# Performance work log

Hardware: AMD Instinct MI355X
Metric: run time of the kernel (lower is better)

Reference implementation:

```python
import jax, jax.numpy as jnp
import numpy as np

N, M, F, W = 600000, 300000, 128, 256  # points, masked points, grid feat_dim, net width


def _lin_init(k, fi, fo):
    k1, k2 = jax.random.split(k)
    s = 1.0 / np.sqrt(fi)
    return (jax.random.uniform(k1, (fi, fo), jnp.float32, -s, s),
            jax.random.uniform(k2, (fo,), jnp.float32, -s, s))


def setup_inputs() -> dict:
    key = jax.random.key(0)
    ks = jax.random.split(key, 24)
    # unique sorted indices emulate the boolean target_mask (static count M)
    idx = jnp.asarray(np.sort(np.random.RandomState(0).permutation(N)[:M]).astype(np.int32))
    inp = {
        "rays_pts_emb": jax.random.normal(ks[0], (N, 3), jnp.float32),
        "rotations_emb": jax.random.normal(ks[1], (N, 4), jnp.float32),
        "shs_emb": jax.random.normal(ks[2], (N, 16, 3), jnp.float32),
        "time_emb": jax.random.uniform(ks[3], (N, 1), jnp.float32),
        "h_emb": jax.random.uniform(ks[4], (N, 1), jnp.float32),
        "grid_sp": jax.random.normal(ks[5], (M, F), jnp.float32),
        "grid_st": jax.random.normal(ks[6], (M, F), jnp.float32),
        "idx": idx,
    }
    layers = [("sp", F, W), ("st", F, W), ("p1", W, W), ("p2", W, 9),
              ("r1", W, W), ("r2", W, 4), ("s1", W, W), ("s2", W, 48),
              ("w1", W, W), ("w2", W, 1), ("m1", W, W), ("m2", W, 1)]
    for i, (nm, fi, fo) in enumerate(layers):
        Wt, b = _lin_init(ks[7 + i], fi, fo)
        inp["W_" + nm] = Wt
        inp["b_" + nm] = b
    return inp


def _head(x, W1, b1, W2, b2):
    # nn.Sequential(ReLU, Linear, ReLU, Linear)
    h = jax.nn.relu(x)
    h = jax.nn.relu(h @ W1 + b1)
    return h @ W2 + b2


def reference(rays_pts_emb, rotations_emb, shs_emb, time_emb, h_emb, grid_sp, grid_st, idx,
              W_sp, b_sp, W_st, b_st, W_p1, b_p1, W_p2, b_p2, W_r1, b_r1, W_r2, b_r2,
              W_s1, b_s1, W_s2, b_s2, W_w1, b_w1, W_w2, b_w2, W_m1, b_m1, W_m2, b_m2):
    # encoders (Linear only, no activation)
    sp = grid_sp @ W_sp + b_sp            # [M, W]
    st = grid_st @ W_st + b_st            # [M, W]
    t = time_emb[0:1]                     # [1, 1]
    mint = 1.0 - t
    # position deformation: Bezier combination of 3 control offsets
    dx = _head(sp, W_p1, b_p1, W_p2, b_p2).reshape(-1, 3, 3)  # [M, 3, 3]
    delta = (3.0 * mint ** 2 * t * dx[:, 0]
             + 3.0 * mint * t ** 2 * dx[:, 1]
             + t ** 3 * dx[:, 2])                              # [M, 3]
    pts = rays_pts_emb.at[idx].add(delta)
    rotations = rotations_emb.at[idx].add(_head(st, W_r1, b_r1, W_r2, b_r2))
    shs = shs_emb.at[idx].add(_head(st, W_s1, b_s1, W_s2, b_s2).reshape(-1, 16, 3))
    # opacity gating
    w = _head(sp, W_w1, b_w1, W_w2, b_w2) ** 2                 # [M, 1]
    mu = jax.nn.sigmoid(_head(sp, W_m1, b_m1, W_m2, b_m2))     # [M, 1]
    opacity = h_emb.at[idx].set(h_emb[idx] * jnp.exp(-w * (t - mu) ** 2))
    return (pts, rotations, opacity, shs)
```

## Files before the change

### kernel.cpp

```cpp
#include <hip/hip_runtime.h>
#include <hip/hip_bf16.h>
#include <stdint.h>

#define M_ROWS 300000

typedef __attribute__((ext_vector_type(8)))  short bf16x8;
typedef __attribute__((ext_vector_type(16))) float f32x16;

union U4 { uint4 u; bf16x8 h; unsigned short us[8]; };

__device__ __forceinline__ unsigned short f2bf(float f) {
  union { float f; uint32_t u; } v; v.f = f;
  uint32_t r = v.u + 0x7fffu + ((v.u >> 16) & 1u);
  return (unsigned short)(r >> 16);
}

#define T_SP 0
#define T_ST 64
#define T_P1 128
#define T_P2 256
#define T_R1 272
#define T_R2 400
#define T_S1 416
#define T_S2 544
#define T_W1 576
#define T_W2 704
#define T_M1 720
#define T_M2 848
#define T_TOT 864

__global__ void prep_w(const float* Wsp, const float* Wst, const float* Wp1, const float* Wp2,
                       const float* Wr1, const float* Wr2, const float* Ws1, const float* Ws2,
                       const float* Ww1, const float* Ww2, const float* Wm1, const float* Wm2,
                       uint4* ws) {
  int b = blockIdx.x, l = threadIdx.x;
  const int starts[12] = {T_SP,T_ST,T_P1,T_P2,T_R1,T_R2,T_S1,T_S2,T_W1,T_W2,T_M1,T_M2};
  const int Ks[12]     = {128,128,256,256,256,256,256,256,256,256,256,256};
  const int Cos[12]    = {256,256,256,9,256,4,256,48,256,1,256,1};
  const float* Wp[12]  = {Wsp,Wst,Wp1,Wp2,Wr1,Wr2,Ws1,Ws2,Ww1,Ww2,Wm1,Wm2};
  int m = 0;
  #pragma unroll
  for (int i = 1; i < 12; ++i) if (b >= starts[i]) m = i;
  int local = b - starts[m];
  int KT = Ks[m] >> 4;
  int n0 = local / KT, k0 = local - n0 * KT;
  int col = n0 * 32 + (l & 31);
  int kbase = k0 * 16 + (l >> 5) * 8;
  const float* W = Wp[m];
  int Co = Cos[m];
  U4 pk;
  #pragma unroll
  for (int j = 0; j < 8; ++j) {
    float v = (col < Co) ? W[(size_t)(kbase + j) * Co + col] : 0.0f;
    pk.us[j] = f2bf(v);
  }
  ws[(size_t)b * 64 + l] = pk.u;
}

__global__ void copy_emb(const float4* pts, const float4* rot, const float4* h,
                         const float4* shs, float4* out) {
  long long stride = (long long)gridDim.x * blockDim.x;
  for (long long i = (long long)blockIdx.x * blockDim.x + threadIdx.x; i < 8400000LL; i += stride) {
    float4 v;
    if (i < 450000)        v = pts[i];
    else if (i < 1050000)  v = rot[i - 450000];
    else if (i < 1200000)  v = h[i - 1050000];
    else                   v = shs[i - 1200000];
    out[i] = v;
  }
}

#define LSTR 512
__device__ __forceinline__ int lds_addr(int row, int cb) {
  return row * LSTR + (cb ^ ((row & 15) << 4));
}

__device__ __forceinline__ void loadX(const float* grid, int row0, int t, char* buf) {
  #pragma unroll
  for (int i = 0; i < 4; ++i) {
    int fi = i * 512 + t;
    int row = fi >> 5;
    int c4 = fi & 31;
    int gr = row0 + row; gr = gr < M_ROWS ? gr : (M_ROWS - 1);
    float4 v = ((const float4*)grid)[(size_t)gr * 32 + c4];
    ushort4 p;
    p.x = f2bf(v.x); p.y = f2bf(v.y); p.z = f2bf(v.z); p.w = f2bf(v.w);
    *(ushort4*)(buf + lds_addr(row, c4 * 8)) = p;
  }
}

__device__ __forceinline__ void pre8(U4 (&d)[8], const uint4* base, int lane) {
  #pragma unroll
  for (int i = 0; i < 8; ++i) d[i].u = base[(size_t)i * 64 + lane];
}
__device__ __forceinline__ void pre4(U4 (&d)[8], const uint4* base, int lane) {
  #pragma unroll
  for (int i = 0; i < 4; ++i) d[i].u = base[(size_t)i * 64 + lane];
}
__device__ __forceinline__ void pre_s2(U4 (&d)[8], const uint4* wt, int kq, int lane) {
  #pragma unroll
  for (int kk = 0; kk < 4; ++kk)
    #pragma unroll
    for (int n = 0; n < 2; ++n)
      d[kk * 2 + n].u = wt[(size_t)((n * 16 + kq * 4 + kk) * 64) + lane];
}

__device__ __forceinline__ void mm_big8(U4 (&b)[8], const char* inb, int k0, int arow, int khalf,
                                        f32x16& acc0, f32x16& acc1) {
  #pragma unroll
  for (int k = 0; k < 8; ++k) {
    bf16x8 a0 = *(const bf16x8*)(inb + lds_addr(arow, (k0 + k) * 32 + khalf));
    bf16x8 a1 = *(const bf16x8*)(inb + lds_addr(32 + arow, (k0 + k) * 32 + khalf));
    acc0 = __builtin_amdgcn_mfma_f32_32x32x16_bf16(a0, b[k].h, acc0, 0, 0, 0);
    acc1 = __builtin_amdgcn_mfma_f32_32x32x16_bf16(a1, b[k].h, acc1, 0, 0, 0);
  }
}

__device__ __forceinline__ void store_act(char* outb, const float* bias, int wave, int lane,
                                          const f32x16& acc0, const f32x16& acc1) {
  const int col = wave * 32 + (lane & 31);
  const float bv = bias[col];
  #pragma unroll
  for (int q = 0; q < 16; ++q) {
    int row = (q & 3) + 8 * (q >> 2) + 4 * (lane >> 5);
    float v0 = acc0[q] + bv; v0 = fmaxf(v0, 0.0f);
    float v1 = acc1[q] + bv; v1 = fmaxf(v1, 0.0f);
    *(unsigned short*)(outb + lds_addr(row, col * 2)) = f2bf(v0);
    *(unsigned short*)(outb + lds_addr(32 + row, col * 2)) = f2bf(v1);
  }
}

__device__ __forceinline__ void mm_head1(U4 (&b)[8], const char* inb, int rg, int kq, int khalf,
                                         int lane, f32x16& acc) {
  const int arow = rg * 32 + (lane & 31);
  #pragma unroll
  for (int kk = 0; kk < 4; ++kk) {
    bf16x8 a = *(const bf16x8*)(inb + lds_addr(arow, (kq * 4 + kk) * 32 + khalf));
    acc = __builtin_amdgcn_mfma_f32_32x32x16_bf16(a, b[kk].h, acc, 0, 0, 0);
  }
}
__device__ __forceinline__ void mm_head2(U4 (&b)[8], const char* inb, int rg, int kq, int khalf,
                                         int lane, f32x16& acc0, f32x16& acc1) {
  const int arow = rg * 32 + (lane & 31);
  #pragma unroll
  for (int kk = 0; kk < 4; ++kk) {
    bf16x8 a = *(const bf16x8*)(inb + lds_addr(arow, (kq * 4 + kk) * 32 + khalf));
    acc0 = __builtin_amdgcn_mfma_f32_32x32x16_bf16(a, b[kk * 2 + 0].h, acc0, 0, 0, 0);
    acc1 = __builtin_amdgcn_mfma_f32_32x32x16_bf16(a, b[kk * 2 + 1].h, acc1, 0, 0, 0);
  }
}

template<int COLS>
__device__ __forceinline__ void head_atomic(float* outsm, int rg, int lane, const f32x16& acc) {
  int col = lane & 31;
  if (col < COLS) {
    #pragma unroll
    for (int q = 0; q < 16; ++q) {
      int row = rg * 32 + (q & 3) + 8 * (q >> 2) + 4 * (lane >> 5);
      atomicAdd(&outsm[row * COLS + col], acc[q]);
    }
  }
}
__device__ __forceinline__ void head_atomic48(float* outsm, int rg, int lane,
                                              const f32x16& a0, const f32x16& a1) {
  int c = lane & 31;
  #pragma unroll
  for (int q = 0; q < 16; ++q) {
    int row = rg * 32 + (q & 3) + 8 * (q >> 2) + 4 * (lane >> 5);
    atomicAdd(&outsm[row * 48 + c], a0[q]);
    if (c < 16) atomicAdd(&outsm[row * 48 + 32 + c], a1[q]);
  }
}

__global__ void __launch_bounds__(512, 4) deform_main(
    const float* grid_sp, const float* grid_st, const int* idx,
    const float* rays, const float* rotq, const float* shs_in,
    const float* time_emb, const float* h_emb,
    const uint4* ws,
    const float* b_sp, const float* b_st, const float* b_p1, const float* b_p2,
    const float* b_r1, const float* b_r2, const float* b_s1, const float* b_s2,
    const float* b_w1, const float* b_w2, const float* b_m1, const float* b_m2,
    float* out) {
  __shared__ char bufA[32768];
  __shared__ char bufB[32768];
  __shared__ float sm[3456];
  float* dxb  = sm;
  float* shsb = sm;
  float* wb   = sm + 3072;
  float* mub  = sm + 3136;
  float* rotb = sm + 3200;

  const int t = threadIdx.x;
  const int lane = t & 63;
  const int wave = t >> 6;
  const int rg = wave & 1;
  const int kq = wave >> 1;
  const int arow = lane & 31;
  const int khalf = (lane >> 5) * 16;
  const int row0 = blockIdx.x * 64;
  const float tt = time_emb[0];

  U4 b0[8], b1[8];
  pre8(b0, ws + (size_t)(T_SP + wave * 8) * 64, lane);

  for (int i = t; i < 576; i += 512) dxb[i] = 0.0f;
  for (int i = 3072 + t; i < 3456; i += 512) sm[i] = 0.0f;
  loadX(grid_sp, row0, t, bufA);
  __syncthreads();

  {
    f32x16 a0 = (f32x16)0.0f, a1 = (f32x16)0.0f;
    pre8(b1, ws + (size_t)(T_P1 + wave * 16) * 64, lane);
    mm_big8(b0, bufA, 0, arow, khalf, a0, a1);
    store_act(bufB, b_sp, wave, lane, a0, a1);
  }
  __syncthreads();

  {
    f32x16 a0 = (f32x16)0.0f, a1 = (f32x16)0.0f;
    pre8(b0, ws + (size_t)(T_P1 + wave * 16 + 8) * 64, lane);
    mm_big8(b1, bufB, 0, arow, khalf, a0, a1);
    pre4(b1, ws + (size_t)(T_P2 + kq * 4) * 64, lane);
    mm_big8(b0, bufB, 8, arow, khalf, a0, a1);
    store_act(bufA, b_p1, wave, lane, a0, a1);
  }
  __syncthreads();

  {
    f32x16 hacc = (f32x16)0.0f;
    pre8(b0, ws + (size_t)(T_W1 + wave * 16) * 64, lane);
    mm_head1(b1, bufA, rg, kq, khalf, lane, hacc);
    head_atomic<9>(dxb, rg, lane, hacc);
  }
  __syncthreads();

  {
    f32x16 a0 = (f32x16)0.0f, a1 = (f32x16)0.0f;
    pre8(b1, ws + (size_t)(T_W1 + wave * 16 + 8) * 64, lane);
    mm_big8(b0, bufB, 0, arow, khalf, a0, a1);
    pre4(b0, ws + (size_t)(T_W2 + kq * 4) * 64, lane);
    mm_big8(b1, bufB, 8, arow, khalf, a0, a1);
    store_act(bufA, b_w1, wave, lane, a0, a1);
  }
  __syncthreads();

  {
    f32x16 hacc = (f32x16)0.0f;
    pre8(b1, ws + (size_t)(T_M1 + wave * 16) * 64, lane);
    mm_head1(b0, bufA, rg, kq, khalf, lane, hacc);
    head_atomic<1>(wb, rg, lane, hacc);
  }
  __syncthreads();

  {
    f32x16 a0 = (f32x16)0.0f, a1 = (f32x16)0.0f;
    pre8(b0, ws + (size_t)(T_M1 + wave * 16 + 8) * 64, lane);
    mm_big8(b1, bufB, 0, arow, khalf, a0, a1);
    pre4(b1, ws + (size_t)(T_M2 + kq * 4) * 64, lane);
    mm_big8(b0, bufB, 8, arow, khalf, a0, a1);
    store_act(bufA, b_m1, wave, lane, a0, a1);
  }
  __syncthreads();

  {
    f32x16 hacc = (f32x16)0.0f;
    pre8(b0, ws + (size_t)(T_ST + wave * 8) * 64, lane);
    mm_head1(b1, bufA, rg, kq, khalf, lane, hacc);
    head_atomic<1>(mub, rg, lane, hacc);
  }
  __syncthreads();

  loadX(grid_st, row0, t, bufA);
  if (t < 256) {
    int row = t >> 2, sub = t & 3;
    int gr = row0 + row;
    if (gr < M_ROWS) {
      int g = idx[gr];
      if (sub < 3) {
        float mt = 1.0f - tt;
        float c0 = 3.0f * mt * mt * tt, c1 = 3.0f * mt * tt * tt, c2 = tt * tt * tt;
        float d0 = dxb[row * 9 + sub]     + b_p2[sub];
        float d1 = dxb[row * 9 + 3 + sub] + b_p2[3 + sub];
        float d2 = dxb[row * 9 + 6 + sub] + b_p2[6 + sub];
        out[(size_t)g * 3 + sub] = rays[(size_t)g * 3 + sub] + (c0 * d0 + c1 * d1 + c2 * d2);
      } else {
        float wr = wb[row] + b_w2[0];
        float mr = mub[row] + b_m2[0];
        float mu = 1.0f / (1.0f + expf(-mr));
        float dtm = tt - mu;
        out[4200000 + (size_t)g] = h_emb[g] * expf(-(wr * wr) * dtm * dtm);
      }
    }
  }
  __syncthreads();

  {
    f32x16 a0 = (f32x16)0.0f, a1 = (f32x16)0.0f;
    pre8(b1, ws + (size_t)(T_R1 + wave * 16) * 64, lane);
    mm_big8(b0, bufA, 0, arow, khalf, a0, a1);
    store_act(bufB, b_st, wave, lane, a0, a1);
  }
  __syncthreads();

  {
    f32x16 a0 = (f32x16)0.0f, a1 = (f32x16)0.0f;
    pre8(b0, ws + (size_t)(T_R1 + wave * 16 + 8) * 64, lane);
    mm_big8(b1, bufB, 0, arow, khalf, a0, a1);
    pre4(b1, ws + (size_t)(T_R2 + kq * 4) * 64, lane);
    mm_big8(b0, bufB, 8, arow, khalf, a0, a1);
    store_act(bufA, b_r1, wave, lane, a0, a1);
  }
  __syncthreads();

  {
    f32x16 hacc = (f32x16)0.0f;
    pre8(b0, ws + (size_t)(T_S1 + wave * 16) * 64, lane);
    mm_head1(b1, bufA, rg, kq, khalf, lane, hacc);
    for (int i = t; i < 3072; i += 512) shsb[i] = 0.0f;
    head_atomic<4>(rotb, rg, lane, hacc);
  }
  __syncthreads();

  {
    f32x16 a0 = (f32x16)0.0f, a1 = (f32x16)0.0f;
    pre8(b1, ws + (size_t)(T_S1 + wave * 16 + 8) * 64, lane);
    mm_big8(b0, bufB, 0, arow, khalf, a0, a1);
    pre_s2(b0, ws + (size_t)T_S2 * 64, kq, lane);
    mm_big8(b1, bufB, 8, arow, khalf, a0, a1);
    store_act(bufA, b_s1, wave, lane, a0, a1);
    if (t < 256) {
      int row = t >> 2, c = t & 3;
      int gr = row0 + row;
      if (gr < M_ROWS) {
        int g = idx[gr];
        out[1800000 + (size_t)g * 4 + c] = rotq[(size_t)g * 4 + c] + rotb[row * 4 + c] + b_r2[c];
      }
    }
  }
  __syncthreads();

  {
    f32x16 h0 = (f32x16)0.0f, h1 = (f32x16)0.0f;
    mm_head2(b0, bufA, rg, kq, khalf, lane, h0, h1);
    head_atomic48(shsb, rg, lane, h0, h1);
  }
  __syncthreads();

  #pragma unroll
  for (int i = 0; i < 6; ++i) {
    int e = i * 512 + t;
    int row = e / 48;
    int c = e - row * 48;
    int gr = row0 + row;
    if (gr < M_ROWS) {
      int g = idx[gr];
      out[4800000 + (size_t)g * 48 + c] = shs_in[(size_t)g * 48 + c] + shsb[e] + b_s2[c];
    }
  }
}

extern "C" void kernel_launch(void* const* d_in, const int* in_sizes, int n_in,
                              void* d_out, int out_size, void* d_ws, size_t ws_size,
                              hipStream_t stream) {
  const float* rays     = (const float*)d_in[0];
  const float* rotq     = (const float*)d_in[1];
  const float* shs      = (const float*)d_in[2];
  const float* time_emb = (const float*)d_in[3];
  const float* h_emb    = (const float*)d_in[4];
  const float* grid_sp  = (const float*)d_in[5];
  const float* grid_st  = (const float*)d_in[6];
  const int*   idx      = (const int*)d_in[7];
  uint4* ws = (uint4*)d_ws;

  prep_w<<<T_TOT, 64, 0, stream>>>(
      (const float*)d_in[8],  (const float*)d_in[10], (const float*)d_in[12], (const float*)d_in[14],
      (const float*)d_in[16], (const float*)d_in[18], (const float*)d_in[20], (const float*)d_in[22],
      (const float*)d_in[24], (const float*)d_in[26], (const float*)d_in[28], (const float*)d_in[30],
      ws);

  copy_emb<<<2048, 256, 0, stream>>>((const float4*)rays, (const float4*)rotq,
                                     (const float4*)h_emb, (const float4*)shs, (float4*)d_out);

  deform_main<<<(M_ROWS + 63) / 64, 512, 0, stream>>>(
      grid_sp, grid_st, idx, rays, rotq, shs, time_emb, h_emb, ws,
      (const float*)d_in[9],  (const float*)d_in[11], (const float*)d_in[13], (const float*)d_in[15],
      (const float*)d_in[17], (const float*)d_in[19], (const float*)d_in[21], (const float*)d_in[23],
      (const float*)d_in[25], (const float*)d_in[27], (const float*)d_in[29], (const float*)d_in[31],
      (float*)d_out);
}
```

Measured before the change: 802.1 us.

## Fuse width-1 opacity heads into hidden-layer epilogue and vectorize scatter writes

```diff
diff --git a/kernel.cpp b/kernel.cpp
--- a/kernel.cpp
+++ b/kernel.cpp
@@ -130,65 +130,45 @@
   }
 }
 
-__device__ __forceinline__ void mm_head1(U4 (&b)[8], const char* inb, int rg, int kq, int khalf,
-                                         int lane, f32x16& acc) {
+__device__ __forceinline__ f32x16 mm_head1(U4 (&b)[8], const char* inb, int rg, int kq, int khalf,
+                                           int lane) {
   const int arow = rg * 32 + (lane & 31);
-  #pragma unroll
-  for (int kk = 0; kk < 4; ++kk) {
-    bf16x8 a = *(const bf16x8*)(inb + lds_addr(arow, (kq * 4 + kk) * 32 + khalf));
-    acc = __builtin_amdgcn_mfma_f32_32x32x16_bf16(a, b[kk].h, acc, 0, 0, 0);
-  }
-}
-__device__ __forceinline__ void mm_head2(U4 (&b)[8], const char* inb, int rg, int kq, int khalf,
-                                         int lane, f32x16& acc0, f32x16& acc1) {
-  const int arow = rg * 32 + (lane & 31);
-  #pragma unroll
-  for (int kk = 0; kk < 4; ++kk) {
-    bf16x8 a = *(const bf16x8*)(inb + lds_addr(arow, (kq * 4 + kk) * 32 + khalf));
-    acc0 = __builtin_amdgcn_mfma_f32_32x32x16_bf16(a, b[kk * 2 + 0].h, acc0, 0, 0, 0);
-    acc1 = __builtin_amdgcn_mfma_f32_32x32x16_bf16(a, b[kk * 2 + 1].h, acc1, 0, 0, 0);
-  }
-}
-
-template<int COLS>
-__device__ __forceinline__ void head_atomic(float* outsm, int rg, int lane, const f32x16& acc) {
-  int col = lane & 31;
-  if (col < COLS) {
-    #pragma unroll
-    for (int q = 0; q < 16; ++q) {
-      int row = rg * 32 + (q & 3) + 8 * (q >> 2) + 4 * (lane >> 5);
-      atomicAdd(&outsm[row * COLS + col], acc[q]);
-    }
-  }
-}
-__device__ __forceinline__ void head_atomic48(float* outsm, int rg, int lane,
-                                              const f32x16& a0, const f32x16& a1) {
-  int c = lane & 31;
-  #pragma unroll
-  for (int q = 0; q < 16; ++q) {
-    int row = rg * 32 + (q & 3) + 8 * (q >> 2) + 4 * (lane >> 5);
-    atomicAdd(&outsm[row * 48 + c], a0[q]);
-    if (c < 16) atomicAdd(&outsm[row * 48 + 32 + c], a1[q]);
-  }
+  f32x16 hA = (f32x16)0.0f, hB = (f32x16)0.0f;
+  bf16x8 a0 = *(const bf16x8*)(inb + lds_addr(arow, (kq * 4 + 0) * 32 + khalf));
+  bf16x8 a1 = *(const bf16x8*)(inb + lds_addr(arow, (kq * 4 + 1) * 32 + khalf));
+  bf16x8 a2 = *(const bf16x8*)(inb + lds_addr(arow, (kq * 4 + 2) * 32 + khalf));
+  bf16x8 a3 = *(const bf16x8*)(inb + lds_addr(arow, (kq * 4 + 3) * 32 + khalf));
+  hA = __builtin_amdgcn_mfma_f32_32x32x16_bf16(a0, b[0].h, hA, 0, 0, 0);
+  hB = __builtin_amdgcn_mfma_f32_32x32x16_bf16(a1, b[1].h, hB, 0, 0, 0);
+  hA = __builtin_amdgcn_mfma_f32_32x32x16_bf16(a2, b[2].h, hA, 0, 0, 0);
+  hB = __builtin_amdgcn_mfma_f32_32x32x16_bf16(a3, b[3].h, hB, 0, 0, 0);
+  return hA + hB;
+}
+
+__device__ __forceinline__ float red32(float v) {
+  v += __shfl_xor(v, 1);  v += __shfl_xor(v, 2);  v += __shfl_xor(v, 4);
+  v += __shfl_xor(v, 8);  v += __shfl_xor(v, 16);
+  return v;
 }
 
 __global__ void __launch_bounds__(512, 4) deform_main(
     const float* grid_sp, const float* grid_st, const int* idx,
     const float* rays, const float* rotq, const float* shs_in,
     const float* time_emb, const float* h_emb,
-    const uint4* ws,
+    const uint4* ws, const float* Ww2f, const float* Wm2f,
     const float* b_sp, const float* b_st, const float* b_p1, const float* b_p2,
     const float* b_r1, const float* b_r2, const float* b_s1, const float* b_s2,
     const float* b_w1, const float* b_w2, const float* b_m1, const float* b_m2,
     float* out) {
   __shared__ char bufA[32768];
   __shared__ char bufB[32768];
-  __shared__ float sm[3456];
-  float* dxb  = sm;
+  __shared__ float sm[3584];
+  __shared__ int sidx[64];
   float* shsb = sm;
-  float* wb   = sm + 3072;
-  float* mub  = sm + 3136;
-  float* rotb = sm + 3200;
+  float* dxp  = sm;
+  float* wp   = sm + 2304;
+  float* mup  = sm + 2816;
+  float* rotb = sm + 3328;
 
   const int t = threadIdx.x;
   const int lane = t & 63;
@@ -203,15 +183,17 @@
   U4 b0[8], b1[8];
   pre8(b0, ws + (size_t)(T_SP + wave * 8) * 64, lane);
 
-  for (int i = t; i < 576; i += 512) dxb[i] = 0.0f;
-  for (int i = 3072 + t; i < 3456; i += 512) sm[i] = 0.0f;
+  if (t < 64) { int gr = row0 + t; sidx[t] = idx[gr < M_ROWS ? gr : (M_ROWS - 1)]; }
+  if (t < 256) rotb[t] = 0.0f;
   loadX(grid_sp, row0, t, bufA);
   __syncthreads();
 
   {
     f32x16 a0 = (f32x16)0.0f, a1 = (f32x16)0.0f;
     pre8(b1, ws + (size_t)(T_P1 + wave * 16) * 64, lane);
+    __builtin_amdgcn_s_setprio(1);
     mm_big8(b0, bufA, 0, arow, khalf, a0, a1);
+    __builtin_amdgcn_s_setprio(0);
     store_act(bufB, b_sp, wave, lane, a0, a1);
   }
   __syncthreads();
@@ -219,54 +201,78 @@
   {
     f32x16 a0 = (f32x16)0.0f, a1 = (f32x16)0.0f;
     pre8(b0, ws + (size_t)(T_P1 + wave * 16 + 8) * 64, lane);
+    __builtin_amdgcn_s_setprio(1);
     mm_big8(b1, bufB, 0, arow, khalf, a0, a1);
+    __builtin_amdgcn_s_setprio(0);
     pre4(b1, ws + (size_t)(T_P2 + kq * 4) * 64, lane);
+    __builtin_amdgcn_s_setprio(1);
     mm_big8(b0, bufB, 8, arow, khalf, a0, a1);
+    __builtin_amdgcn_s_setprio(0);
     store_act(bufA, b_p1, wave, lane, a0, a1);
   }
   __syncthreads();
 
   {
-    f32x16 hacc = (f32x16)0.0f;
     pre8(b0, ws + (size_t)(T_W1 + wave * 16) * 64, lane);
-    mm_head1(b1, bufA, rg, kq, khalf, lane, hacc);
-    head_atomic<9>(dxb, rg, lane, hacc);
+    f32x16 h = mm_head1(b1, bufA, rg, kq, khalf, lane);
+    int col = lane & 31;
+    if (col < 9) {
+      #pragma unroll
+      for (int q = 0; q < 16; ++q) {
+        int row = rg * 32 + (q & 3) + 8 * (q >> 2) + 4 * (lane >> 5);
+        dxp[(kq * 64 + row) * 9 + col] = h[q];
+      }
+    }
   }
   __syncthreads();
 
   {
     f32x16 a0 = (f32x16)0.0f, a1 = (f32x16)0.0f;
     pre8(b1, ws + (size_t)(T_W1 + wave * 16 + 8) * 64, lane);
+    __builtin_amdgcn_s_setprio(1);
     mm_big8(b0, bufB, 0, arow, khalf, a0, a1);
-    pre4(b0, ws + (size_t)(T_W2 + kq * 4) * 64, lane);
+    __builtin_amdgcn_s_setprio(0);
+    pre8(b0, ws + (size_t)(T_M1 + wave * 16) * 64, lane);
+    __builtin_amdgcn_s_setprio(1);
     mm_big8(b1, bufB, 8, arow, khalf, a0, a1);
-    store_act(bufA, b_w1, wave, lane, a0, a1);
-  }
-  __syncthreads();
-
-  {
-    f32x16 hacc = (f32x16)0.0f;
-    pre8(b1, ws + (size_t)(T_M1 + wave * 16) * 64, lane);
-    mm_head1(b0, bufA, rg, kq, khalf, lane, hacc);
-    head_atomic<1>(wb, rg, lane, hacc);
-  }
-  __syncthreads();
-
-  {
-    f32x16 a0 = (f32x16)0.0f, a1 = (f32x16)0.0f;
-    pre8(b0, ws + (size_t)(T_M1 + wave * 16 + 8) * 64, lane);
-    mm_big8(b1, bufB, 0, arow, khalf, a0, a1);
-    pre4(b1, ws + (size_t)(T_M2 + kq * 4) * 64, lane);
-    mm_big8(b0, bufB, 8, arow, khalf, a0, a1);
-    store_act(bufA, b_m1, wave, lane, a0, a1);
-  }
-  __syncthreads();
-
-  {
-    f32x16 hacc = (f32x16)0.0f;
+    __builtin_amdgcn_s_setprio(0);
+    const int hcol = wave * 32 + (lane & 31);
+    const float bv = b_w1[hcol], wv = Ww2f[hcol];
+    #pragma unroll
+    for (int q = 0; q < 16; ++q) {
+      int row = (q & 3) + 8 * (q >> 2) + 4 * (lane >> 5);
+      float s0 = red32(fmaxf(a0[q] + bv, 0.0f) * wv);
+      float s1 = red32(fmaxf(a1[q] + bv, 0.0f) * wv);
+      if ((lane & 31) == 0) { wp[wave * 64 + row] = s0; wp[wave * 64 + 32 + row] = s1; }
+    }
+  }
+  __syncthreads();
+
+  float pr = 0.0f, hv = 0.0f;
+  {
+    if (t < 256) {
+      int row = t >> 2, sub = t & 3;
+      int g = sidx[row];
+      if (sub < 3) pr = rays[(size_t)g * 3 + sub]; else hv = h_emb[g];
+    }
+    f32x16 a0 = (f32x16)0.0f, a1 = (f32x16)0.0f;
+    pre8(b1, ws + (size_t)(T_M1 + wave * 16 + 8) * 64, lane);
+    __builtin_amdgcn_s_setprio(1);
+    mm_big8(b0, bufB, 0, arow, khalf, a0, a1);
+    __builtin_amdgcn_s_setprio(0);
     pre8(b0, ws + (size_t)(T_ST + wave * 8) * 64, lane);
-    mm_head1(b1, bufA, rg, kq, khalf, lane, hacc);
-    head_atomic<1>(mub, rg, lane, hacc);
+    __builtin_amdgcn_s_setprio(1);
+    mm_big8(b1, bufB, 8, arow, khalf, a0, a1);
+    __builtin_amdgcn_s_setprio(0);
+    const int hcol = wave * 32 + (lane & 31);
+    const float bv = b_m1[hcol], wv = Wm2f[hcol];
+    #pragma unroll
+    for (int q = 0; q < 16; ++q) {
+      int row = (q & 3) + 8 * (q >> 2) + 4 * (lane >> 5);
+      float s0 = red32(fmaxf(a0[q] + bv, 0.0f) * wv);
+      float s1 = red32(fmaxf(a1[q] + bv, 0.0f) * wv);
+      if ((lane & 31) == 0) { mup[wave * 64 + row] = s0; mup[wave * 64 + 32 + row] = s1; }
+    }
   }
   __syncthreads();
 
@@ -275,20 +281,24 @@
     int row = t >> 2, sub = t & 3;
     int gr = row0 + row;
     if (gr < M_ROWS) {
-      int g = idx[gr];
+      int g = sidx[row];
       if (sub < 3) {
         float mt = 1.0f - tt;
         float c0 = 3.0f * mt * mt * tt, c1 = 3.0f * mt * tt * tt, c2 = tt * tt * tt;
-        float d0 = dxb[row * 9 + sub]     + b_p2[sub];
-        float d1 = dxb[row * 9 + 3 + sub] + b_p2[3 + sub];
-        float d2 = dxb[row * 9 + 6 + sub] + b_p2[6 + sub];
-        out[(size_t)g * 3 + sub] = rays[(size_t)g * 3 + sub] + (c0 * d0 + c1 * d1 + c2 * d2);
+        float d0 = b_p2[sub],     d1 = b_p2[3 + sub], d2 = b_p2[6 + sub];
+        #pragma unroll
+        for (int k = 0; k < 4; ++k) {
+          const float* dp = &dxp[(k * 64 + row) * 9];
+          d0 += dp[sub]; d1 += dp[3 + sub]; d2 += dp[6 + sub];
+        }
+        out[(size_t)g * 3 + sub] = pr + (c0 * d0 + c1 * d1 + c2 * d2);
       } else {
-        float wr = wb[row] + b_w2[0];
-        float mr = mub[row] + b_m2[0];
+        float wr = b_w2[0], mr = b_m2[0];
+        #pragma unroll
+        for (int w8 = 0; w8 < 8; ++w8) { wr += wp[w8 * 64 + row]; mr += mup[w8 * 64 + row]; }
         float mu = 1.0f / (1.0f + expf(-mr));
         float dtm = tt - mu;
-        out[4200000 + (size_t)g] = h_emb[g] * expf(-(wr * wr) * dtm * dtm);
+        out[4200000 + (size_t)g] = hv * expf(-(wr * wr) * dtm * dtm);
       }
     }
   }
@@ -297,7 +307,9 @@
   {
     f32x16 a0 = (f32x16)0.0f, a1 = (f32x16)0.0f;
     pre8(b1, ws + (size_t)(T_R1 + wave * 16) * 64, lane);
+    __builtin_amdgcn_s_setprio(1);
     mm_big8(b0, bufA, 0, arow, khalf, a0, a1);
+    __builtin_amdgcn_s_setprio(0);
     store_act(bufB, b_st, wave, lane, a0, a1);
   }
   __syncthreads();
@@ -305,56 +317,100 @@
   {
     f32x16 a0 = (f32x16)0.0f, a1 = (f32x16)0.0f;
     pre8(b0, ws + (size_t)(T_R1 + wave * 16 + 8) * 64, lane);
+    __builtin_amdgcn_s_setprio(1);
     mm_big8(b1, bufB, 0, arow, khalf, a0, a1);
+    __builtin_amdgcn_s_setprio(0);
     pre4(b1, ws + (size_t)(T_R2 + kq * 4) * 64, lane);
+    __builtin_amdgcn_s_setprio(1);
     mm_big8(b0, bufB, 8, arow, khalf, a0, a1);
+    __builtin_amdgcn_s_setprio(0);
     store_act(bufA, b_r1, wave, lane, a0, a1);
   }
   __syncthreads();
 
-  {
-    f32x16 hacc = (f32x16)0.0f;
+  float4 rq;
+  {
+    if (t < 64) rq = ((const float4*)rotq)[sidx[t]];
     pre8(b0, ws + (size_t)(T_S1 + wave * 16) * 64, lane);
-    mm_head1(b1, bufA, rg, kq, khalf, lane, hacc);
-    for (int i = t; i < 3072; i += 512) shsb[i] = 0.0f;
-    head_atomic<4>(rotb, rg, lane, hacc);
+    f32x16 h = mm_head1(b1, bufA, rg, kq, khalf, lane);
+    int col = lane & 31;
+    if (col < 4) {
+      #pragma unroll
+      for (int q = 0; q < 16; ++q) {
+        int row = rg * 32 + (q & 3) + 8 * (q >> 2) + 4 * (lane >> 5);
+        atomicAdd(&rotb[row * 4 + col], h[q]);
+      }
+    }
   }
   __syncthreads();
 
   {
     f32x16 a0 = (f32x16)0.0f, a1 = (f32x16)0.0f;
     pre8(b1, ws + (size_t)(T_S1 + wave * 16 + 8) * 64, lane);
+    __builtin_amdgcn_s_setprio(1);
     mm_big8(b0, bufB, 0, arow, khalf, a0, a1);
+    __builtin_amdgcn_s_setprio(0);
     pre_s2(b0, ws + (size_t)T_S2 * 64, kq, lane);
+    __builtin_amdgcn_s_setprio(1);
     mm_big8(b1, bufB, 8, arow, khalf, a0, a1);
+    __builtin_amdgcn_s_setprio(0);
     store_act(bufA, b_s1, wave, lane, a0, a1);
+    #pragma unroll
+    for (int i = 0; i < 6; ++i) shsb[i * 512 + t] = 0.0f;
+    if (t < 64 && row0 + t < M_ROWS) {
+      int g = sidx[t];
+      float4 o;
+      o.x = rq.x + rotb[t * 4 + 0] + b_r2[0];
+      o.y = rq.y + rotb[t * 4 + 1] + b_r2[1];
+      o.z = rq.z + rotb[t * 4 + 2] + b_r2[2];
+      o.w = rq.w + rotb[t * 4 + 3] + b_r2[3];
+      ((float4*)out)[450000 + (size_t)g] = o;
+    }
+  }
+  __syncthreads();
+
+  float4 sv0, sv1;
+  int r0v = t / 12, c40 = t - r0v * 12;
+  int e1 = 512 + t, r1v = e1 / 12, c41 = e1 - r1v * 12;
+  {
+    sv0 = ((const float4*)shs_in)[(size_t)sidx[r0v] * 12 + c40];
+    if (t < 256) sv1 = ((const float4*)shs_in)[(size_t)sidx[r1v] * 12 + c41];
+    f32x16 h0 = (f32x16)0.0f, h1 = (f32x16)0.0f;
+    const int ar = rg * 32 + (lane & 31);
+    #pragma unroll
+    for (int kk = 0; kk < 4; ++kk) {
+      bf16x8 a = *(const bf16x8*)(bufA + lds_addr(ar, (kq * 4 + kk) * 32 + khalf));
+      h0 = __builtin_amdgcn_mfma_f32_32x32x16_bf16(a, b0[kk * 2 + 0].h, h0, 0, 0, 0);
+      h1 = __builtin_amdgcn_mfma_f32_32x32x16_bf16(a, b0[kk * 2 + 1].h, h1, 0, 0, 0);
+    }
+    int c = lane & 31;
+    #pragma unroll
+    for (int q = 0; q < 16; ++q) {
+      int row = rg * 32 + (q & 3) + 8 * (q >> 2) + 4 * (lane >> 5);
+      atomicAdd(&shsb[row * 48 + c], h0[q]);
+      if (c < 16) atomicAdd(&shsb[row * 48 + 32 + c], h1[q]);
+    }
+  }
+  __syncthreads();
+
+  {
+    float4 bias0 = ((const float4*)b_s2)[c40];
+    float4 acc0 = ((const float4*)shsb)[r0v * 12 + c40];
+    if (row0 + r0v < M_ROWS) {
+      float4 o;
+      o.x = sv0.x + acc0.x + bias0.x; o.y = sv0.y + acc0.y + bias0.y;
+      o.z = sv0.z + acc0.z + bias0.z; o.w = sv0.w + acc0.w + bias0.w;
+      ((float4*)out)[1200000 + (size_t)sidx[r0v] * 12 + c40] = o;
+    }
     if (t < 256) {
-      int row = t >> 2, c = t & 3;
-      int gr = row0 + row;
-      if (gr < M_ROWS) {
-        int g = idx[gr];
-        out[1800000 + (size_t)g * 4 + c] = rotq[(size_t)g * 4 + c] + rotb[row * 4 + c] + b_r2[c];
+      float4 bias1 = ((const float4*)b_s2)[c41];
+      float4 acc1 = ((const float4*)shsb)[r1v * 12 + c41];
+      if (row0 + r1v < M_ROWS) {
+        float4 o;
+        o.x = sv1.x + acc1.x + bias1.x; o.y = sv1.y + acc1.y + bias1.y;
+        o.z = sv1.z + acc1.z + bias1.z; o.w = sv1.w + acc1.w + bias1.w;
+        ((float4*)out)[1200000 + (size_t)sidx[r1v] * 12 + c41] = o;
       }
-    }
-  }
-  __syncthreads();
-
-  {
-    f32x16 h0 = (f32x16)0.0f, h1 = (f32x16)0.0f;
-    mm_head2(b0, bufA, rg, kq, khalf, lane, h0, h1);
-    head_atomic48(shsb, rg, lane, h0, h1);
-  }
-  __syncthreads();
-
-  #pragma unroll
-  for (int i = 0; i < 6; ++i) {
-    int e = i * 512 + t;
-    int row = e / 48;
-    int c = e - row * 48;
-    int gr = row0 + row;
-    if (gr < M_ROWS) {
-      int g = idx[gr];
-      out[4800000 + (size_t)g * 48 + c] = shs_in[(size_t)g * 48 + c] + shsb[e] + b_s2[c];
     }
   }
 }
@@ -383,6 +439,7 @@
 
   deform_main<<<(M_ROWS + 63) / 64, 512, 0, stream>>>(
       grid_sp, grid_st, idx, rays, rotq, shs, time_emb, h_emb, ws,
+      (const float*)d_in[26], (const float*)d_in[30],
       (const float*)d_in[9],  (const float*)d_in[11], (const float*)d_in[13], (const float*)d_in[15],
       (const float*)d_in[17], (const float*)d_in[19], (const float*)d_in[21], (const float*)d_in[23],
       (const float*)d_in[25], (const float*)d_in[27], (const float*)d_in[29], (const float*)d_in[31],
```

Result: slower. 1.094 ms (+36.4%).

## Split sp and st branches into separate blocks with prefetched gathers

Applied to the files above, without the earlier changes.

```diff
diff --git a/kernel.cpp b/kernel.cpp
--- a/kernel.cpp
+++ b/kernel.cpp
@@ -139,16 +139,6 @@
     acc = __builtin_amdgcn_mfma_f32_32x32x16_bf16(a, b[kk].h, acc, 0, 0, 0);
   }
 }
-__device__ __forceinline__ void mm_head2(U4 (&b)[8], const char* inb, int rg, int kq, int khalf,
-                                         int lane, f32x16& acc0, f32x16& acc1) {
-  const int arow = rg * 32 + (lane & 31);
-  #pragma unroll
-  for (int kk = 0; kk < 4; ++kk) {
-    bf16x8 a = *(const bf16x8*)(inb + lds_addr(arow, (kq * 4 + kk) * 32 + khalf));
-    acc0 = __builtin_amdgcn_mfma_f32_32x32x16_bf16(a, b[kk * 2 + 0].h, acc0, 0, 0, 0);
-    acc1 = __builtin_amdgcn_mfma_f32_32x32x16_bf16(a, b[kk * 2 + 1].h, acc1, 0, 0, 0);
-  }
-}
 
 template<int COLS>
 __device__ __forceinline__ void head_atomic(float* outsm, int rg, int lane, const f32x16& acc) {
@@ -183,12 +173,13 @@
     float* out) {
   __shared__ char bufA[32768];
   __shared__ char bufB[32768];
-  __shared__ float sm[3456];
-  float* dxb  = sm;
-  float* shsb = sm;
-  float* wb   = sm + 3072;
-  float* mub  = sm + 3136;
-  float* rotb = sm + 3200;
+  __shared__ float smf[3456];
+  __shared__ int sidx[64];
+  float* dxb  = smf;
+  float* shsb = smf;
+  float* wb   = smf + 3072;
+  float* mub  = smf + 3136;
+  float* rotb = smf + 3200;
 
   const int t = threadIdx.x;
   const int lane = t & 63;
@@ -197,164 +188,200 @@
   const int kq = wave >> 1;
   const int arow = lane & 31;
   const int khalf = (lane >> 5) * 16;
-  const int row0 = blockIdx.x * 64;
+  const int path = blockIdx.x & 1;
+  const int row0 = (blockIdx.x >> 1) * 64;
   const float tt = time_emb[0];
 
   U4 b0[8], b1[8];
-  pre8(b0, ws + (size_t)(T_SP + wave * 8) * 64, lane);
-
-  for (int i = t; i < 576; i += 512) dxb[i] = 0.0f;
-  for (int i = 3072 + t; i < 3456; i += 512) sm[i] = 0.0f;
-  loadX(grid_sp, row0, t, bufA);
-  __syncthreads();
-
-  {
-    f32x16 a0 = (f32x16)0.0f, a1 = (f32x16)0.0f;
-    pre8(b1, ws + (size_t)(T_P1 + wave * 16) * 64, lane);
-    mm_big8(b0, bufA, 0, arow, khalf, a0, a1);
-    store_act(bufB, b_sp, wave, lane, a0, a1);
-  }
-  __syncthreads();
-
-  {
-    f32x16 a0 = (f32x16)0.0f, a1 = (f32x16)0.0f;
-    pre8(b0, ws + (size_t)(T_P1 + wave * 16 + 8) * 64, lane);
-    mm_big8(b1, bufB, 0, arow, khalf, a0, a1);
-    pre4(b1, ws + (size_t)(T_P2 + kq * 4) * 64, lane);
-    mm_big8(b0, bufB, 8, arow, khalf, a0, a1);
-    store_act(bufA, b_p1, wave, lane, a0, a1);
-  }
-  __syncthreads();
-
-  {
-    f32x16 hacc = (f32x16)0.0f;
-    pre8(b0, ws + (size_t)(T_W1 + wave * 16) * 64, lane);
-    mm_head1(b1, bufA, rg, kq, khalf, lane, hacc);
-    head_atomic<9>(dxb, rg, lane, hacc);
-  }
-  __syncthreads();
-
-  {
-    f32x16 a0 = (f32x16)0.0f, a1 = (f32x16)0.0f;
-    pre8(b1, ws + (size_t)(T_W1 + wave * 16 + 8) * 64, lane);
-    mm_big8(b0, bufB, 0, arow, khalf, a0, a1);
-    pre4(b0, ws + (size_t)(T_W2 + kq * 4) * 64, lane);
-    mm_big8(b1, bufB, 8, arow, khalf, a0, a1);
-    store_act(bufA, b_w1, wave, lane, a0, a1);
-  }
-  __syncthreads();
-
-  {
-    f32x16 hacc = (f32x16)0.0f;
-    pre8(b1, ws + (size_t)(T_M1 + wave * 16) * 64, lane);
-    mm_head1(b0, bufA, rg, kq, khalf, lane, hacc);
-    head_atomic<1>(wb, rg, lane, hacc);
-  }
-  __syncthreads();
-
-  {
-    f32x16 a0 = (f32x16)0.0f, a1 = (f32x16)0.0f;
-    pre8(b0, ws + (size_t)(T_M1 + wave * 16 + 8) * 64, lane);
-    mm_big8(b1, bufB, 0, arow, khalf, a0, a1);
-    pre4(b1, ws + (size_t)(T_M2 + kq * 4) * 64, lane);
-    mm_big8(b0, bufB, 8, arow, khalf, a0, a1);
-    store_act(bufA, b_m1, wave, lane, a0, a1);
-  }
-  __syncthreads();
-
-  {
-    f32x16 hacc = (f32x16)0.0f;
-    pre8(b0, ws + (size_t)(T_ST + wave * 8) * 64, lane);
-    mm_head1(b1, bufA, rg, kq, khalf, lane, hacc);
-    head_atomic<1>(mub, rg, lane, hacc);
-  }
-  __syncthreads();
-
-  loadX(grid_st, row0, t, bufA);
-  if (t < 256) {
-    int row = t >> 2, sub = t & 3;
-    int gr = row0 + row;
-    if (gr < M_ROWS) {
-      int g = idx[gr];
-      if (sub < 3) {
-        float mt = 1.0f - tt;
-        float c0 = 3.0f * mt * mt * tt, c1 = 3.0f * mt * tt * tt, c2 = tt * tt * tt;
-        float d0 = dxb[row * 9 + sub]     + b_p2[sub];
-        float d1 = dxb[row * 9 + 3 + sub] + b_p2[3 + sub];
-        float d2 = dxb[row * 9 + 6 + sub] + b_p2[6 + sub];
-        out[(size_t)g * 3 + sub] = rays[(size_t)g * 3 + sub] + (c0 * d0 + c1 * d1 + c2 * d2);
-      } else {
-        float wr = wb[row] + b_w2[0];
-        float mr = mub[row] + b_m2[0];
-        float mu = 1.0f / (1.0f + expf(-mr));
-        float dtm = tt - mu;
-        out[4200000 + (size_t)g] = h_emb[g] * expf(-(wr * wr) * dtm * dtm);
-      }
-    }
-  }
-  __syncthreads();
-
-  {
-    f32x16 a0 = (f32x16)0.0f, a1 = (f32x16)0.0f;
-    pre8(b1, ws + (size_t)(T_R1 + wave * 16) * 64, lane);
-    mm_big8(b0, bufA, 0, arow, khalf, a0, a1);
-    store_act(bufB, b_st, wave, lane, a0, a1);
-  }
-  __syncthreads();
-
-  {
-    f32x16 a0 = (f32x16)0.0f, a1 = (f32x16)0.0f;
-    pre8(b0, ws + (size_t)(T_R1 + wave * 16 + 8) * 64, lane);
-    mm_big8(b1, bufB, 0, arow, khalf, a0, a1);
-    pre4(b1, ws + (size_t)(T_R2 + kq * 4) * 64, lane);
-    mm_big8(b0, bufB, 8, arow, khalf, a0, a1);
-    store_act(bufA, b_r1, wave, lane, a0, a1);
-  }
-  __syncthreads();
-
-  {
-    f32x16 hacc = (f32x16)0.0f;
-    pre8(b0, ws + (size_t)(T_S1 + wave * 16) * 64, lane);
-    mm_head1(b1, bufA, rg, kq, khalf, lane, hacc);
-    for (int i = t; i < 3072; i += 512) shsb[i] = 0.0f;
-    head_atomic<4>(rotb, rg, lane, hacc);
-  }
-  __syncthreads();
-
-  {
-    f32x16 a0 = (f32x16)0.0f, a1 = (f32x16)0.0f;
-    pre8(b1, ws + (size_t)(T_S1 + wave * 16 + 8) * 64, lane);
-    mm_big8(b0, bufB, 0, arow, khalf, a0, a1);
-    pre_s2(b0, ws + (size_t)T_S2 * 64, kq, lane);
-    mm_big8(b1, bufB, 8, arow, khalf, a0, a1);
-    store_act(bufA, b_s1, wave, lane, a0, a1);
+
+  if (t < 64) { int gr = row0 + t; sidx[t] = idx[gr < M_ROWS ? gr : (M_ROWS - 1)]; }
+
+  if (path == 0) {
+    pre8(b0, ws + (size_t)(T_SP + wave * 8) * 64, lane);
+    if (t < 512) dxb[t] = 0.0f;
+    if (t < 64) dxb[512 + t] = 0.0f;
+    if (t < 128) smf[3072 + t] = 0.0f;
+    loadX(grid_sp, row0, t, bufA);
+    __syncthreads();
+
+    {
+      f32x16 a0 = (f32x16)0.0f, a1 = (f32x16)0.0f;
+      pre8(b1, ws + (size_t)(T_P1 + wave * 16) * 64, lane);
+      mm_big8(b0, bufA, 0, arow, khalf, a0, a1);
+      store_act(bufB, b_sp, wave, lane, a0, a1);
+    }
+    __syncthreads();
+
+    {
+      f32x16 a0 = (f32x16)0.0f, a1 = (f32x16)0.0f;
+      pre8(b0, ws + (size_t)(T_P1 + wave * 16 + 8) * 64, lane);
+      mm_big8(b1, bufB, 0, arow, khalf, a0, a1);
+      pre4(b1, ws + (size_t)(T_P2 + kq * 4) * 64, lane);
+      mm_big8(b0, bufB, 8, arow, khalf, a0, a1);
+      store_act(bufA, b_p1, wave, lane, a0, a1);
+    }
+    __syncthreads();
+
+    {
+      f32x16 hacc = (f32x16)0.0f;
+      pre8(b0, ws + (size_t)(T_W1 + wave * 16) * 64, lane);
+      mm_head1(b1, bufA, rg, kq, khalf, lane, hacc);
+      head_atomic<9>(dxb, rg, lane, hacc);
+    }
+    __syncthreads();
+
+    {
+      f32x16 a0 = (f32x16)0.0f, a1 = (f32x16)0.0f;
+      pre8(b1, ws + (size_t)(T_W1 + wave * 16 + 8) * 64, lane);
+      mm_big8(b0, bufB, 0, arow, khalf, a0, a1);
+      pre4(b0, ws + (size_t)(T_W2 + kq * 4) * 64, lane);
+      mm_big8(b1, bufB, 8, arow, khalf, a0, a1);
+      store_act(bufA, b_w1, wave, lane, a0, a1);
+    }
+    __syncthreads();
+
+    {
+      f32x16 hacc = (f32x16)0.0f;
+      pre8(b1, ws + (size_t)(T_M1 + wave * 16) * 64, lane);
+      mm_head1(b0, bufA, rg, kq, khalf, lane, hacc);
+      head_atomic<1>(wb, rg, lane, hacc);
+    }
+    __syncthreads();
+
+    {
+      f32x16 a0 = (f32x16)0.0f, a1 = (f32x16)0.0f;
+      pre8(b0, ws + (size_t)(T_M1 + wave * 16 + 8) * 64, lane);
+      mm_big8(b1, bufB, 0, arow, khalf, a0, a1);
+      pre4(b1, ws + (size_t)(T_M2 + kq * 4) * 64, lane);
+      mm_big8(b0, bufB, 8, arow, khalf, a0, a1);
+      store_act(bufA, b_m1, wave, lane, a0, a1);
+    }
+    __syncthreads();
+
+    float pr = 0.0f, hv = 0.0f;
+    {
+      if (t < 256) {
+        int row = t >> 2, sub = t & 3;
+        int g = sidx[row];
+        if (sub < 3) pr = rays[(size_t)g * 3 + sub]; else hv = h_emb[g];
+      }
+      f32x16 hacc = (f32x16)0.0f;
+      mm_head1(b1, bufA, rg, kq, khalf, lane, hacc);
+      head_atomic<1>(mub, rg, lane, hacc);
+    }
+    __syncthreads();
+
     if (t < 256) {
-      int row = t >> 2, c = t & 3;
+      int row = t >> 2, sub = t & 3;
       int gr = row0 + row;
       if (gr < M_ROWS) {
-        int g = idx[gr];
-        out[1800000 + (size_t)g * 4 + c] = rotq[(size_t)g * 4 + c] + rotb[row * 4 + c] + b_r2[c];
-      }
-    }
-  }
-  __syncthreads();
-
-  {
-    f32x16 h0 = (f32x16)0.0f, h1 = (f32x16)0.0f;
-    mm_head2(b0, bufA, rg, kq, khalf, lane, h0, h1);
-    head_atomic48(shsb, rg, lane, h0, h1);
-  }
-  __syncthreads();
-
-  #pragma unroll
-  for (int i = 0; i < 6; ++i) {
-    int e = i * 512 + t;
-    int row = e / 48;
-    int c = e - row * 48;
-    int gr = row0 + row;
-    if (gr < M_ROWS) {
-      int g = idx[gr];
-      out[4800000 + (size_t)g * 48 + c] = shs_in[(size_t)g * 48 + c] + shsb[e] + b_s2[c];
+        int g = sidx[row];
+        if (sub < 3) {
+          float mt = 1.0f - tt;
+          float c0 = 3.0f * mt * mt * tt, c1 = 3.0f * mt * tt * tt, c2 = tt * tt * tt;
+          float d0 = dxb[row * 9 + sub]     + b_p2[sub];
+          float d1 = dxb[row * 9 + 3 + sub] + b_p2[3 + sub];
+          float d2 = dxb[row * 9 + 6 + sub] + b_p2[6 + sub];
+          out[(size_t)g * 3 + sub] = pr + (c0 * d0 + c1 * d1 + c2 * d2);
+        } else {
+          float wr = wb[row] + b_w2[0];
+          float mr = mub[row] + b_m2[0];
+          float mu = 1.0f / (1.0f + expf(-mr));
+          float dtm = tt - mu;
+          out[4200000 + (size_t)g] = hv * expf(-(wr * wr) * dtm * dtm);
+        }
+      }
+    }
+  } else {
+    pre8(b0, ws + (size_t)(T_ST + wave * 8) * 64, lane);
+    #pragma unroll
+    for (int i = 0; i < 6; ++i) shsb[i * 512 + t] = 0.0f;
+    if (t < 256) rotb[t] = 0.0f;
+    loadX(grid_st, row0, t, bufA);
+    __syncthreads();
+
+    {
+      f32x16 a0 = (f32x16)0.0f, a1 = (f32x16)0.0f;
+      pre8(b1, ws + (size_t)(T_R1 + wave * 16) * 64, lane);
+      mm_big8(b0, bufA, 0, arow, khalf, a0, a1);
+      store_act(bufB, b_st, wave, lane, a0, a1);
+    }
+    __syncthreads();
+
+    {
+      f32x16 a0 = (f32x16)0.0f, a1 = (f32x16)0.0f;
+      pre8(b0, ws + (size_t)(T_R1 + wave * 16 + 8) * 64, lane);
+      mm_big8(b1, bufB, 0, arow, khalf, a0, a1);
+      pre4(b1, ws + (size_t)(T_R2 + kq * 4) * 64, lane);
+      mm_big8(b0, bufB, 8, arow, khalf, a0, a1);
+      store_act(bufA, b_r1, wave, lane, a0, a1);
+    }
+    __syncthreads();
+
+    float4 rq;
+    {
+      if (t < 64) rq = ((const float4*)rotq)[sidx[t]];
+      f32x16 hacc = (f32x16)0.0f;
+      pre8(b0, ws + (size_t)(T_S1 + wave * 16) * 64, lane);
+      mm_head1(b1, bufA, rg, kq, khalf, lane, hacc);
+      head_atomic<4>(rotb, rg, lane, hacc);
+    }
+    __syncthreads();
+
+    {
+      f32x16 a0 = (f32x16)0.0f, a1 = (f32x16)0.0f;
+      pre8(b1, ws + (size_t)(T_S1 + wave * 16 + 8) * 64, lane);
+      mm_big8(b0, bufB, 0, arow, khalf, a0, a1);
+      pre_s2(b0, ws + (size_t)T_S2 * 64, kq, lane);
+      mm_big8(b1, bufB, 8, arow, khalf, a0, a1);
+      store_act(bufA, b_s1, wave, lane, a0, a1);
+      if (t < 64 && row0 + t < M_ROWS) {
+        int g = sidx[t];
+        float4 o;
+        o.x = rq.x + rotb[t * 4 + 0] + b_r2[0];
+        o.y = rq.y + rotb[t * 4 + 1] + b_r2[1];
+        o.z = rq.z + rotb[t * 4 + 2] + b_r2[2];
+        o.w = rq.w + rotb[t * 4 + 3] + b_r2[3];
+        ((float4*)out)[450000 + (size_t)g] = o;
+      }
+    }
+    __syncthreads();
+
+    float4 sv0, sv1;
+    int r0v = t / 12, c40 = t - r0v * 12;
+    int e1 = 512 + t, r1v = e1 / 12, c41 = e1 - r1v * 12;
+    {
+      sv0 = ((const float4*)shs_in)[(size_t)sidx[r0v] * 12 + c40];
+      if (t < 256) sv1 = ((const float4*)shs_in)[(size_t)sidx[r1v] * 12 + c41];
+      f32x16 h0 = (f32x16)0.0f, h1 = (f32x16)0.0f;
+      const int ar = rg * 32 + (lane & 31);
+      #pragma unroll
+      for (int kk = 0; kk < 4; ++kk) {
+        bf16x8 a = *(const bf16x8*)(bufA + lds_addr(ar, (kq * 4 + kk) * 32 + khalf));
+        h0 = __builtin_amdgcn_mfma_f32_32x32x16_bf16(a, b0[kk * 2 + 0].h, h0, 0, 0, 0);
+        h1 = __builtin_amdgcn_mfma_f32_32x32x16_bf16(a, b0[kk * 2 + 1].h, h1, 0, 0, 0);
+      }
+      head_atomic48(shsb, rg, lane, h0, h1);
+    }
+    __syncthreads();
+
+    {
+      if (row0 + r0v < M_ROWS) {
+        float4 bias0 = ((const float4*)b_s2)[c40];
+        float4 acc0 = ((const float4*)shsb)[r0v * 12 + c40];
+        float4 o;
+        o.x = sv0.x + acc0.x + bias0.x; o.y = sv0.y + acc0.y + bias0.y;
+        o.z = sv0.z + acc0.z + bias0.z; o.w = sv0.w + acc0.w + bias0.w;
+        ((float4*)out)[1200000 + (size_t)sidx[r0v] * 12 + c40] = o;
+      }
+      if (t < 256 && row0 + r1v < M_ROWS) {
+        float4 bias1 = ((const float4*)b_s2)[c41];
+        float4 acc1 = ((const float4*)shsb)[r1v * 12 + c41];
+        float4 o;
+        o.x = sv1.x + acc1.x + bias1.x; o.y = sv1.y + acc1.y + bias1.y;
+        o.z = sv1.z + acc1.z + bias1.z; o.w = sv1.w + acc1.w + bias1.w;
+        ((float4*)out)[1200000 + (size_t)sidx[r1v] * 12 + c41] = o;
+      }
     }
   }
 }
@@ -381,7 +408,7 @@
   copy_emb<<<2048, 256, 0, stream>>>((const float4*)rays, (const float4*)rotq,
                                      (const float4*)h_emb, (const float4*)shs, (float4*)d_out);
 
-  deform_main<<<(M_ROWS + 63) / 64, 512, 0, stream>>>(
+  deform_main<<<9376, 512, 0, stream>>>(
       grid_sp, grid_st, idx, rays, rotq, shs, time_emb, h_emb, ws,
       (const float*)d_in[9],  (const float*)d_in[11], (const float*)d_in[13], (const float*)d_in[15],
       (const float*)d_in[17], (const float*)d_in[19], (const float*)d_in[21], (const float*)d_in[23],
```

After: 907.3 us. 1.13x slower.
